# Performance work log

Hardware: AMD Instinct MI355X
Metric: run time of the kernel (lower is better)

Reference implementation:

```python
import jax, jax.numpy as jnp
import numpy as np

# Constants from __init__ (domain bounds)
X_MIN, X_MAX = -1.0, 1.0
Y_MIN, Y_MAX = -1.0, 1.0
T_MIN, T_MAX = 0.0, 1.0

N_POINTS = 262144
WIDTH = 128
N_HIDDEN_STACK = 5  # hidden->hidden layers between first and last


def setup_inputs() -> dict:
    key = jax.random.key(0)
    ks = jax.random.split(key, 8)
    X = jax.random.uniform(ks[0], (N_POINTS, 4), dtype=jnp.float32)
    # glorot_normal-ish init
    def glorot(k, fan_in, fan_out, shape):
        std = (2.0 / (fan_in + fan_out)) ** 0.5
        return jax.random.normal(k, shape, dtype=jnp.float32) * std
    W0 = glorot(ks[1], 4, WIDTH, (4, WIDTH))
    b0 = jnp.zeros((WIDTH,), dtype=jnp.float32)
    Wh = glorot(ks[2], WIDTH, WIDTH, (N_HIDDEN_STACK, WIDTH, WIDTH))
    bh = jnp.zeros((N_HIDDEN_STACK, WIDTH), dtype=jnp.float32)
    WL = glorot(ks[3], WIDTH, 2, (WIDTH, 2))
    bL = jnp.zeros((2,), dtype=jnp.float32)
    nu_min = jnp.zeros((), dtype=jnp.float32)
    nu_max = jnp.ones((), dtype=jnp.float32)
    return {"X": X, "nu_min": nu_min, "nu_max": nu_max,
            "W0": W0, "b0": b0, "Wh": Wh, "bh": bh, "WL": WL, "bL": bL}


def _swish(x):
    return x * jax.nn.sigmoid(x)


def reference(X, nu_min, nu_max, W0, b0, Wh, bh, WL, bL):
    # Input rescaling to [-1, 1] per feature, then concat
    x_s = 2.0 * (X[:, 0:1] - X_MIN) / (X_MAX - X_MIN) - 1.0
    y_s = 2.0 * (X[:, 1:2] - Y_MIN) / (Y_MAX - Y_MIN) - 1.0
    t_s = 2.0 * (X[:, 2:3] - T_MIN) / (T_MAX - T_MIN) - 1.0
    nu_s = 2.0 * (X[:, 3:4] - nu_min) / (nu_max - nu_min) - 1.0
    H = jnp.concatenate([x_s, y_s, t_s, nu_s], axis=1)  # [N, 4]
    # Stacked small dense + swish layers (fused-MLP candidate)
    H = _swish(H @ W0 + b0)  # [N, WIDTH]
    for i in range(Wh.shape[0]):
        H = _swish(H @ Wh[i] + bh[i])
    return H @ WL + bL  # [N, 2], no activation on output layer
```

## Files before the change

kernel.cpp:

```cpp
#include <hip/hip_runtime.h>

typedef __bf16 bf16x8 __attribute__((ext_vector_type(8)));
typedef __bf16 bf16x2 __attribute__((ext_vector_type(2)));
typedef float  f32x4  __attribute__((ext_vector_type(4)));

#define WS_WT0_B 0
#define WS_WTH_B 8192
#define WS_WLT_B 172032

__device__ __forceinline__ unsigned short f2b(float f) {
  return __builtin_bit_cast(unsigned short, (__bf16)f);
}

__global__ void prep_kernel(const float* __restrict__ W0,
                            const float* __restrict__ Wh,
                            const float* __restrict__ WL,
                            unsigned short* __restrict__ ws) {
  int i = blockIdx.x * 256 + threadIdx.x;
  int l  = (i >> 3) & 63;
  int j  = i & 7;
  int lm = l & 15, lh = l >> 4;
  if (i < 4096) {
    int nt = i >> 9;
    int n = nt * 16 + lm, k = lh * 8 + j;
    ws[i] = f2b(k < 4 ? W0[k * 128 + n] : 0.f);
  } else if (i < 86016) {
    int t = i - 4096;
    int frag = t >> 9;
    int nt = frag & 7, ks = (frag >> 3) & 3, h = frag >> 5;
    int n = nt * 16 + lm, k = ks * 32 + lh * 8 + j;
    ws[i] = f2b(Wh[(h * 128 + k) * 128 + n]);
  } else if (i < 90112) {
    int t = i - 86016;
    int f = t >> 9;
    int k = (f & 3) * 32 + lh * 8 + j;
    ws[i] = f2b((f < 4 && lm < 2) ? WL[k * 2 + lm] : 0.f);
  }
}

__device__ __forceinline__ f32x4 swish4(f32x4 z) {
  f32x4 e;
  e[0] = __expf(-z[0]); e[1] = __expf(-z[1]);
  e[2] = __expf(-z[2]); e[3] = __expf(-z[3]);
  const f32x4 w = e + 1.f;
  f32x4 s;
  s[0] = __builtin_amdgcn_rcpf(w[0]); s[1] = __builtin_amdgcn_rcpf(w[1]);
  s[2] = __builtin_amdgcn_rcpf(w[2]); s[3] = __builtin_amdgcn_rcpf(w[3]);
  return z * s;
}

__device__ __forceinline__ uint2 pack4(f32x4 r) {
  bf16x2 lo = {(__bf16)r[0], (__bf16)r[1]};
  bf16x2 hi = {(__bf16)r[2], (__bf16)r[3]};
  uint2 wv;
  wv.x = __builtin_bit_cast(unsigned int, lo);
  wv.y = __builtin_bit_cast(unsigned int, hi);
  return wv;
}

#define SB() __builtin_amdgcn_sched_barrier(0)
#define GLD(addr) __builtin_bit_cast(bf16x8, *reinterpret_cast<const uint4*>(addr))
#define LRD(addr) __builtin_bit_cast(bf16x8, *reinterpret_cast<const uint4*>(addr))
#define MFMA(a, b, c) __builtin_amdgcn_mfma_f32_16x16x32_bf16((a), (b), (c), 0, 0, 0)

__launch_bounds__(64, 2)
__global__ void mlp_kernel(const float* __restrict__ X,
                           const float* __restrict__ nu_min_p,
                           const float* __restrict__ nu_max_p,
                           const float* __restrict__ b0,
                           const float* __restrict__ bh,
                           const float* __restrict__ bL,
                           const unsigned short* __restrict__ ws,
                           float* __restrict__ out) {
  __shared__ __align__(16) char smem[32 * 256 + 5 * 128 * 4];
  char* Hs = smem;
  float* bias_lds = reinterpret_cast<float*>(smem + 8192);
  const int lane = threadIdx.x;
  const int lm = lane & 15, lh = lane >> 4;
  const int row0 = blockIdx.x * 32;
  const char* ap = reinterpret_cast<const char*>(ws) + lane * 16;
  const int xorm = (lm & 7) << 4;
  const int va0 = lm * 256 + ((lh * 16) ^ xorm);
  const int va1 = va0 + 16 * 256;
  const int wa0 = lm * 256 + ((lh * 8) ^ xorm);
  const int wa1 = wa0 + 16 * 256;

  bf16x8 aL0[8];
#pragma unroll
  for (int nt = 0; nt < 8; ++nt) aL0[nt] = GLD(ap + WS_WT0_B + nt * 1024);
  f32x4 bv0[8];
#pragma unroll
  for (int nt = 0; nt < 8; ++nt)
    bv0[nt] = *reinterpret_cast<const f32x4*>(b0 + nt * 16 + lh * 4);
  float bstg[10];
#pragma unroll
  for (int i = 0; i < 10; ++i) bstg[i] = bh[i * 64 + lane];

  if (lane < 32) {
    const float4 xv = reinterpret_cast<const float4*>(X)[row0 + lane];
    const float numin = nu_min_p[0], numax = nu_max_p[0];
    const float v0 = xv.x;
    const float v1 = xv.y;
    const float v2 = 2.f * xv.z - 1.f;
    const float v3 = 2.f * (xv.w - numin) / (numax - numin) - 1.f;
    uint4 c0;
    c0.x = (unsigned)f2b(v0) | ((unsigned)f2b(v1) << 16);
    c0.y = (unsigned)f2b(v2) | ((unsigned)f2b(v3) << 16);
    c0.z = 0u; c0.w = 0u;
    const uint4 z4 = make_uint4(0u, 0u, 0u, 0u);
    const int xr = (lane & 7) << 4;
    char* rp = Hs + lane * 256;
    *reinterpret_cast<uint4*>(rp + (0  ^ xr)) = c0;
    *reinterpret_cast<uint4*>(rp + (16 ^ xr)) = z4;
    *reinterpret_cast<uint4*>(rp + (32 ^ xr)) = z4;
    *reinterpret_cast<uint4*>(rp + (48 ^ xr)) = z4;
  }
#pragma unroll
  for (int i = 0; i < 10; ++i) bias_lds[i * 64 + lane] = bstg[i];

  f32x4 acc[8][2];
  bf16x8 bfrA[2], bfrB[2];
  bf16x8 aA[8], aB[8];

  bfrA[0] = LRD(Hs + va0);
  bfrA[1] = LRD(Hs + va1);
#pragma unroll
  for (int nt = 0; nt < 8; ++nt) {
    acc[nt][0] = MFMA(aL0[nt], bfrA[0], bv0[nt]);
    acc[nt][1] = MFMA(aL0[nt], bfrA[1], bv0[nt]);
  }
#pragma unroll
  for (int nt = 0; nt < 8; ++nt) aA[nt] = GLD(ap + WS_WTH_B + nt * 1024);
#pragma unroll
  for (int nt = 0; nt < 8; ++nt) {
#pragma unroll
    for (int pt = 0; pt < 2; ++pt) {
      const uint2 wv = pack4(swish4(acc[nt][pt]));
      *reinterpret_cast<uint2*>(Hs + ((pt ? wa1 : wa0) ^ (nt << 5))) = wv;
    }
  }

  const f32x4 zero4 = {0.f, 0.f, 0.f, 0.f};

#pragma unroll 1
  for (int h = 0; h < 5; ++h) {
    const char* wb = ap + WS_WTH_B + h * 32768;
    const float* bl = bias_lds + h * 128;

    bfrA[0] = LRD(Hs + va0);
    bfrA[1] = LRD(Hs + va1);
#pragma unroll
    for (int nt = 0; nt < 8; ++nt) aB[nt] = GLD(wb + 8192 + nt * 1024);
    bfrB[0] = LRD(Hs + (va0 ^ 64));
    bfrB[1] = LRD(Hs + (va1 ^ 64));
#pragma unroll
    for (int nt = 0; nt < 8; ++nt) {
      acc[nt][0] = MFMA(aA[nt], bfrA[0], zero4);
      acc[nt][1] = MFMA(aA[nt], bfrA[1], zero4);
    }
    SB();
#pragma unroll
    for (int nt = 0; nt < 8; ++nt) aA[nt] = GLD(wb + 16384 + nt * 1024);
    bfrA[0] = LRD(Hs + (va0 ^ 128));
    bfrA[1] = LRD(Hs + (va1 ^ 128));
#pragma unroll
    for (int nt = 0; nt < 8; ++nt) {
      acc[nt][0] = MFMA(aB[nt], bfrB[0], acc[nt][0]);
      acc[nt][1] = MFMA(aB[nt], bfrB[1], acc[nt][1]);
    }
    SB();
#pragma unroll
    for (int nt = 0; nt < 8; ++nt) aB[nt] = GLD(wb + 24576 + nt * 1024);
    bfrB[0] = LRD(Hs + (va0 ^ 192));
    bfrB[1] = LRD(Hs + (va1 ^ 192));
#pragma unroll
    for (int nt = 0; nt < 8; ++nt) {
      acc[nt][0] = MFMA(aA[nt], bfrA[0], acc[nt][0]);
      acc[nt][1] = MFMA(aA[nt], bfrA[1], acc[nt][1]);
    }
    SB();
#pragma unroll
    for (int nt = 0; nt < 8; ++nt) aA[nt] = GLD(wb + 32768 + nt * 1024);
#pragma unroll
    for (int nt = 0; nt < 8; ++nt) {
      acc[nt][0] = MFMA(aB[nt], bfrB[0], acc[nt][0]);
      acc[nt][1] = MFMA(aB[nt], bfrB[1], acc[nt][1]);
    }
    SB();
#pragma unroll
    for (int nt = 0; nt < 8; ++nt) {
      const f32x4 bv = *reinterpret_cast<const f32x4*>(bl + nt * 16 + lh * 4);
#pragma unroll
      for (int pt = 0; pt < 2; ++pt) {
        const uint2 wv = pack4(swish4(acc[nt][pt] + bv));
        *reinterpret_cast<uint2*>(Hs + ((pt ? wa1 : wa0) ^ (nt << 5))) = wv;
      }
    }
  }

  {
    const float bl0 = bL[0], bl1 = bL[1];
#pragma unroll
    for (int pt = 0; pt < 2; ++pt) {
      f32x4 accL = {0.f, 0.f, 0.f, 0.f};
#pragma unroll
      for (int ks = 0; ks < 4; ++ks) {
        const bf16x8 bfr = LRD(Hs + ((pt ? va1 : va0) ^ (ks << 6)));
        accL = MFMA(aA[ks], bfr, accL);
      }
      if (lh == 0) {
        const int p = pt * 16 + lm;
        float2 o;
        o.x = accL[0] + bl0;
        o.y = accL[1] + bl1;
        *reinterpret_cast<float2*>(out + (size_t)(row0 + p) * 2) = o;
      }
    }
  }
}

extern "C" void kernel_launch(void* const* d_in, const int* in_sizes, int n_in,
                              void* d_out, int out_size, void* d_ws, size_t ws_size,
                              hipStream_t stream) {
  const float* X     = (const float*)d_in[0];
  const float* numin = (const float*)d_in[1];
  const float* numax = (const float*)d_in[2];
  const float* W0    = (const float*)d_in[3];
  const float* b0    = (const float*)d_in[4];
  const float* Wh    = (const float*)d_in[5];
  const float* bh    = (const float*)d_in[6];
  const float* WL    = (const float*)d_in[7];
  const float* bL    = (const float*)d_in[8];
  unsigned short* ws = (unsigned short*)d_ws;
  float* out = (float*)d_out;

  hipLaunchKernelGGL(prep_kernel, dim3(352), dim3(256), 0, stream, W0, Wh, WL, ws);
  hipLaunchKernelGGL(mlp_kernel, dim3(8192), dim3(64), 0, stream,
                     X, numin, numax, b0, bh, bL, ws, out);
}
```

Baseline: 78.26 us.

## Fold hidden biases into MFMA accumulator init, drop bias LDS, raise occupancy

Hidden-layer biases are now loaded from global memory into registers one layer ahead and used as the initial MFMA accumulator, instead of being staged in LDS and added before swish. This shrinks shared memory to the activation tile only and removes the per-element bias add. The launch bound hint goes from 2 to 3 waves per EU, which caps register use and may cause spills. Swish now computes exp as exp2 with a pre-scaled argument to save a multiply.

```diff
diff --git a/kernel.cpp b/kernel.cpp
--- a/kernel.cpp
+++ b/kernel.cpp
@@ -39,9 +39,15 @@
 }
 
 __device__ __forceinline__ f32x4 swish4(f32x4 z) {
+  const f32x4 u = z * (-1.44269504088896340736f);
   f32x4 e;
-  e[0] = __expf(-z[0]); e[1] = __expf(-z[1]);
-  e[2] = __expf(-z[2]); e[3] = __expf(-z[3]);
+#if __has_builtin(__builtin_amdgcn_exp2f)
+  e[0] = __builtin_amdgcn_exp2f(u[0]); e[1] = __builtin_amdgcn_exp2f(u[1]);
+  e[2] = __builtin_amdgcn_exp2f(u[2]); e[3] = __builtin_amdgcn_exp2f(u[3]);
+#else
+  e[0] = __expf(u[0] * 0.6931471805599453f); e[1] = __expf(u[1] * 0.6931471805599453f);
+  e[2] = __expf(u[2] * 0.6931471805599453f); e[3] = __expf(u[3] * 0.6931471805599453f);
+#endif
   const f32x4 w = e + 1.f;
   f32x4 s;
   s[0] = __builtin_amdgcn_rcpf(w[0]); s[1] = __builtin_amdgcn_rcpf(w[1]);
@@ -63,7 +69,7 @@
 #define LRD(addr) __builtin_bit_cast(bf16x8, *reinterpret_cast<const uint4*>(addr))
 #define MFMA(a, b, c) __builtin_amdgcn_mfma_f32_16x16x32_bf16((a), (b), (c), 0, 0, 0)
 
-__launch_bounds__(64, 2)
+__launch_bounds__(64, 3)
 __global__ void mlp_kernel(const float* __restrict__ X,
                            const float* __restrict__ nu_min_p,
                            const float* __restrict__ nu_max_p,
@@ -72,9 +78,7 @@
                            const float* __restrict__ bL,
                            const unsigned short* __restrict__ ws,
                            float* __restrict__ out) {
-  __shared__ __align__(16) char smem[32 * 256 + 5 * 128 * 4];
-  char* Hs = smem;
-  float* bias_lds = reinterpret_cast<float*>(smem + 8192);
+  __shared__ __align__(16) char Hs[32 * 256];
   const int lane = threadIdx.x;
   const int lm = lane & 15, lh = lane >> 4;
   const int row0 = blockIdx.x * 32;
@@ -88,13 +92,10 @@
   bf16x8 aL0[8];
 #pragma unroll
   for (int nt = 0; nt < 8; ++nt) aL0[nt] = GLD(ap + WS_WT0_B + nt * 1024);
-  f32x4 bv0[8];
+  f32x4 bvh[8];
 #pragma unroll
   for (int nt = 0; nt < 8; ++nt)
-    bv0[nt] = *reinterpret_cast<const f32x4*>(b0 + nt * 16 + lh * 4);
-  float bstg[10];
-#pragma unroll
-  for (int i = 0; i < 10; ++i) bstg[i] = bh[i * 64 + lane];
+    bvh[nt] = *reinterpret_cast<const f32x4*>(b0 + nt * 16 + lh * 4);
 
   if (lane < 32) {
     const float4 xv = reinterpret_cast<const float4*>(X)[row0 + lane];
@@ -115,8 +116,6 @@
     *reinterpret_cast<uint4*>(rp + (32 ^ xr)) = z4;
     *reinterpret_cast<uint4*>(rp + (48 ^ xr)) = z4;
   }
-#pragma unroll
-  for (int i = 0; i < 10; ++i) bias_lds[i * 64 + lane] = bstg[i];
 
   f32x4 acc[8][2];
   bf16x8 bfrA[2], bfrB[2];
@@ -126,9 +125,12 @@
   bfrA[1] = LRD(Hs + va1);
 #pragma unroll
   for (int nt = 0; nt < 8; ++nt) {
-    acc[nt][0] = MFMA(aL0[nt], bfrA[0], bv0[nt]);
-    acc[nt][1] = MFMA(aL0[nt], bfrA[1], bv0[nt]);
-  }
+    acc[nt][0] = MFMA(aL0[nt], bfrA[0], bvh[nt]);
+    acc[nt][1] = MFMA(aL0[nt], bfrA[1], bvh[nt]);
+  }
+#pragma unroll
+  for (int nt = 0; nt < 8; ++nt)
+    bvh[nt] = *reinterpret_cast<const f32x4*>(bh + nt * 16 + lh * 4);
 #pragma unroll
   for (int nt = 0; nt < 8; ++nt) aA[nt] = GLD(ap + WS_WTH_B + nt * 1024);
 #pragma unroll
@@ -140,12 +142,10 @@
     }
   }
 
-  const f32x4 zero4 = {0.f, 0.f, 0.f, 0.f};
-
 #pragma unroll 1
   for (int h = 0; h < 5; ++h) {
     const char* wb = ap + WS_WTH_B + h * 32768;
-    const float* bl = bias_lds + h * 128;
+    const float* bnext = bh + (h == 4 ? 4 : h + 1) * 128;
 
     bfrA[0] = LRD(Hs + va0);
     bfrA[1] = LRD(Hs + va1);
@@ -155,9 +155,12 @@
     bfrB[1] = LRD(Hs + (va1 ^ 64));
 #pragma unroll
     for (int nt = 0; nt < 8; ++nt) {
-      acc[nt][0] = MFMA(aA[nt], bfrA[0], zero4);
-      acc[nt][1] = MFMA(aA[nt], bfrA[1], zero4);
-    }
+      acc[nt][0] = MFMA(aA[nt], bfrA[0], bvh[nt]);
+      acc[nt][1] = MFMA(aA[nt], bfrA[1], bvh[nt]);
+    }
+#pragma unroll
+    for (int nt = 0; nt < 8; ++nt)
+      bvh[nt] = *reinterpret_cast<const f32x4*>(bnext + nt * 16 + lh * 4);
     SB();
 #pragma unroll
     for (int nt = 0; nt < 8; ++nt) aA[nt] = GLD(wb + 16384 + nt * 1024);
@@ -189,10 +192,9 @@
     SB();
 #pragma unroll
     for (int nt = 0; nt < 8; ++nt) {
-      const f32x4 bv = *reinterpret_cast<const f32x4*>(bl + nt * 16 + lh * 4);
 #pragma unroll
       for (int pt = 0; pt < 2; ++pt) {
-        const uint2 wv = pack4(swish4(acc[nt][pt] + bv));
+        const uint2 wv = pack4(swish4(acc[nt][pt]));
         *reinterpret_cast<uint2*>(Hs + ((pt ? wa1 : wa0) ^ (nt << 5))) = wv;
       }
     }
```

Result: slower. 106.6 us (+36.3%).
